# Kernel tuning notes

Measured on AMD Instinct MI355X. Metric: run time of the kernel, lower is better.

The kernel has to match this reference:

```python
import jax, jax.numpy as jnp
import numpy as np

B = 128          # batch
D = 2048         # original_dim
P = 16000        # projection_dim


def _count_sketch_matrix(key, d, p):
    """Dense count-sketch matrix: one +/-1 per row at a random column.
    Mirrors the torch init: col ~ randint(0, p-1), sign = 2*randint(0,2)-1."""
    k_idx, k_sgn = jax.random.split(key)
    idx = jax.random.randint(k_idx, (d,), 0, p - 1)            # torch uses high=p-1 (exclusive)
    sgn = (2 * jax.random.randint(k_sgn, (d,), 0, 2) - 1).astype(jnp.float32)
    C = jnp.zeros((d, p), dtype=jnp.float32)
    return C.at[jnp.arange(d), idx].set(sgn)


def setup_inputs() -> dict:
    key = jax.random.key(0)
    kx1, kx2, kc1, kc2 = jax.random.split(key, 4)
    x1 = jax.random.normal(kx1, (B, D), dtype=jnp.float32)
    x2 = jax.random.normal(kx2, (B, D), dtype=jnp.float32)
    C1 = _count_sketch_matrix(kc1, D, P)
    C2 = _count_sketch_matrix(kc2, D, P)
    return {"x1": x1, "x2": x2, "C1": C1, "C2": C2}


def reference(x1, x2, C1, C2):
    # Count-sketch projections (dense mm, as in the original module)
    y1 = x1 @ C1                      # [B, P]
    y2 = x2 @ C2                      # [B, P]
    # Circular convolution via FFT -> elementwise complex multiply -> IFFT.
    # Original takes only the real part of the IFFT output.
    f1 = jnp.fft.fft(y1, axis=-1)
    f2 = jnp.fft.fft(y2, axis=-1)
    phi = jnp.fft.ifft(f1 * f2, axis=-1).real.astype(jnp.float32)
    return phi                        # [B, P]
```

## Files before the change

### kernel.cpp

```cpp
#include <hip/hip_runtime.h>

#define NFFT 16000
#define BATCH 128
#define DIM 2048

__device__ __forceinline__ float2 cmul(float2 a, float2 b) {
    return make_float2(a.x * b.x - a.y * b.y, a.x * b.y + a.y * b.x);
}

__device__ __forceinline__ int rev5_3(int n) {
    int d0 = n % 5, r = n / 5;
    int d1 = r % 5, d2 = r / 5;
    return d0 * 25 + d1 * 5 + d2;
}

__device__ __forceinline__ int perm_slot(int p) {
    return (p & 127) * 125 + rev5_3(p >> 7);
}

__global__ void gen_twiddles(float2* W) {
    int j = blockIdx.x * blockDim.x + threadIdx.x;
    if (j < NFFT) {
        double a = -2.0 * 3.141592653589793238462643383279502884 * (double)j / (double)NFFT;
        W[j] = make_float2((float)cos(a), (float)sin(a));
    }
}

__global__ void extract_sketch(const float* __restrict__ C1, const float* __restrict__ C2,
                               int* __restrict__ idx1, float* __restrict__ sgn1,
                               int* __restrict__ idx2, float* __restrict__ sgn2) {
    int gwave = (blockIdx.x * blockDim.x + threadIdx.x) >> 6;
    int lane = threadIdx.x & 63;
    if (gwave >= 2 * DIM) return;
    const float* row;
    int* idxp; float* sgnp; int d;
    if (gwave < DIM) { d = gwave;       row = C1 + (size_t)d * NFFT; idxp = idx1; sgnp = sgn1; }
    else             { d = gwave - DIM; row = C2 + (size_t)d * NFFT; idxp = idx2; sgnp = sgn2; }
    for (int it = 0; it < 63; ++it) {
        int off = it * 256 + lane * 4;
        float4 v = make_float4(0.f, 0.f, 0.f, 0.f);
        if (off < NFFT) v = *reinterpret_cast<const float4*>(row + off);
        bool found = (v.x != 0.f) || (v.y != 0.f) || (v.z != 0.f) || (v.w != 0.f);
        if (found) {
            int j; float s;
            if (v.x != 0.f)      { j = 0; s = v.x; }
            else if (v.y != 0.f) { j = 1; s = v.y; }
            else if (v.z != 0.f) { j = 2; s = v.z; }
            else                 { j = 3; s = v.w; }
            idxp[d] = off + j;
            sgnp[d] = s;
        }
        if (__any(found)) break;
    }
}

__device__ void fft16000(float2* ld, const float2* __restrict__ W) {
    const int tid = threadIdx.x;
    const int nt = blockDim.x;
    const float C1_5 = 0.30901699437494742f, S1_5 = 0.95105651629515357f;
    const float C2_5 = -0.80901699437494745f, S2_5 = 0.58778525229247312f;
    const float2 w5tab[5] = { make_float2(1.f, 0.f),
                              make_float2(C1_5, -S1_5), make_float2(C2_5, -S2_5),
                              make_float2(C2_5,  S2_5), make_float2(C1_5,  S1_5) };

    #pragma unroll
    for (int s = 0; s < 3; ++s) {
        const int m = (s == 0) ? 1 : (s == 1) ? 5 : 25;
        const int twmul = NFFT / (5 * m);
        for (int task = tid; task < 128 * 25; task += nt) {
            int n1 = task / 25;
            int bf = task % 25;
            int t = bf % m, blk = bf / m;
            int base = n1 * 125 + blk * (5 * m) + t;
            float2 xv[5];
            #pragma unroll
            for (int r = 0; r < 5; ++r) xv[r] = ld[base + r * m];
            if (m > 1) {
                int step = twmul * t;
                #pragma unroll
                for (int r = 1; r < 5; ++r) xv[r] = cmul(xv[r], W[step * r]);
            }
            float2 y[5];
            #pragma unroll
            for (int q = 0; q < 5; ++q) {
                float2 acc = xv[0];
                #pragma unroll
                for (int r = 1; r < 5; ++r) {
                    float2 t2 = cmul(xv[r], w5tab[(q * r) % 5]);
                    acc.x += t2.x; acc.y += t2.y;
                }
                y[q] = acc;
            }
            #pragma unroll
            for (int q = 0; q < 5; ++q) ld[base + q * m] = y[q];
        }
        __syncthreads();
    }

    for (int idx = tid; idx < NFFT; idx += nt) {
        int n1 = idx / 125;
        int k2 = idx - n1 * 125;
        int rn1 = (int)(__brev((unsigned)n1) >> 25);
        if (n1 > rn1) continue;
        int pb = rn1 * 125 + k2;
        float2 va = ld[idx], vb = ld[pb];
        va = cmul(va, W[n1 * k2]);
        vb = cmul(vb, W[rn1 * k2]);
        ld[idx] = vb;
        ld[pb] = va;
    }
    __syncthreads();

    #pragma unroll
    for (int s = 0; s < 7; ++s) {
        const int m = 1 << s;
        const int twmul = NFFT >> (s + 1);
        for (int task = tid; task < 125 * 64; task += nt) {
            int bf = task / 125;
            int k2 = task - bf * 125;
            int t = bf & (m - 1);
            int blk = bf >> s;
            int pa = (blk * 2 * m + t) * 125 + k2;
            int pb = pa + m * 125;
            float2 a = ld[pa], b = ld[pb];
            float2 wb = cmul(W[twmul * t], b);
            ld[pa] = make_float2(a.x + wb.x, a.y + wb.y);
            ld[pb] = make_float2(a.x - wb.x, a.y - wb.y);
        }
        __syncthreads();
    }
}

__global__ void fused_fft(const float* __restrict__ x1, const float* __restrict__ x2,
                          const int* __restrict__ idx1, const float* __restrict__ sgn1,
                          const int* __restrict__ idx2, const float* __restrict__ sgn2,
                          float* __restrict__ out, const float2* __restrict__ W) {
    extern __shared__ float2 ld[];
    const int b = blockIdx.x;
    const int tid = threadIdx.x, nt = blockDim.x;

    for (int i = tid; i < NFFT; i += nt) ld[i] = make_float2(0.f, 0.f);
    __syncthreads();

    const float* x1b = x1 + (size_t)b * DIM;
    const float* x2b = x2 + (size_t)b * DIM;
    for (int d = tid; d < DIM; d += nt) {
        float v1 = sgn1[d] * x1b[d];
        atomicAdd(&ld[perm_slot(idx1[d])].x, v1);
        float v2 = sgn2[d] * x2b[d];
        atomicAdd(&ld[perm_slot(idx2[d])].y, v2);
    }
    __syncthreads();

    fft16000(ld, W);

    float2 vals[8][2];
    int nk = 0;
    for (int k = tid; k <= NFFT / 2; k += nt) {
        int m = (k == 0) ? 0 : NFFT - k;
        float2 Zk = ld[k], Zm = ld[m];
        float u = (Zk.x * Zk.x - Zk.y * Zk.y) - (Zm.x * Zm.x - Zm.y * Zm.y);
        float v = 2.f * (Zk.x * Zk.y + Zm.x * Zm.y);
        vals[nk][0] = make_float2(0.25f * v,  0.25f * u);
        vals[nk][1] = make_float2(0.25f * v, -0.25f * u);
        ++nk;
    }
    __syncthreads();
    nk = 0;
    for (int k = tid; k <= NFFT / 2; k += nt) {
        ld[perm_slot(k)] = vals[nk][0];
        if (k != 0 && k != NFFT / 2)
            ld[perm_slot(NFFT - k)] = vals[nk][1];
        ++nk;
    }
    __syncthreads();

    fft16000(ld, W);

    const float invN = 1.0f / (float)NFFT;
    float* outb = out + (size_t)b * NFFT;
    for (int k = tid; k < NFFT; k += nt) outb[k] = ld[k].x * invN;
}

extern "C" void kernel_launch(void* const* d_in, const int* in_sizes, int n_in,
                              void* d_out, int out_size, void* d_ws, size_t ws_size,
                              hipStream_t stream) {
    (void)in_sizes; (void)n_in; (void)out_size; (void)ws_size;
    const float* x1 = (const float*)d_in[0];
    const float* x2 = (const float*)d_in[1];
    const float* C1 = (const float*)d_in[2];
    const float* C2 = (const float*)d_in[3];
    float* out = (float*)d_out;

    char* w = (char*)d_ws;
    int*    idx1 = (int*)  (w);
    float*  sgn1 = (float*)(w + 8192);
    int*    idx2 = (int*)  (w + 16384);
    float*  sgn2 = (float*)(w + 24576);
    float2* W    = (float2*)(w + 32768);

    (void)hipFuncSetAttribute((const void*)fused_fft,
                              hipFuncAttributeMaxDynamicSharedMemorySize, NFFT * 8);

    gen_twiddles  <<<63, 256, 0, stream>>>(W);
    extract_sketch<<<(2 * DIM) / 4, 256, 0, stream>>>(C1, C2, idx1, sgn1, idx2, sgn2);
    fused_fft     <<<BATCH, 1024, NFFT * 8, stream>>>(x1, x2, idx1, sgn1, idx2, sgn2, out, W);
}
```

Measured before the change: 356.3 us.

## Restructure FFT into radix-4 stages with on-the-fly twiddles and no reorder pass

Replaces the seven radix-2 stages and the explicit bit-reversal/twiddle permutation pass with three radix-4 stages plus one radix-2 stage, reading output in digit-reversed order via index mapping. Twiddle factors are computed with fast sin/cos intrinsics instead of a global table, removing the twiddle generation kernel. The sketch extraction loads four float4 chunks per step for more memory parallelism. Fast trig intrinsics may reduce accuracy slightly.

```diff
diff --git a/kernel.cpp b/kernel.cpp
--- a/kernel.cpp
+++ b/kernel.cpp
@@ -7,6 +7,9 @@
 __device__ __forceinline__ float2 cmul(float2 a, float2 b) {
     return make_float2(a.x * b.x - a.y * b.y, a.x * b.y + a.y * b.x);
 }
+__device__ __forceinline__ float2 cadd(float2 a, float2 b) { return make_float2(a.x + b.x, a.y + b.y); }
+__device__ __forceinline__ float2 csub(float2 a, float2 b) { return make_float2(a.x - b.x, a.y - b.y); }
+__device__ __forceinline__ float2 cis(float ang) { return make_float2(__cosf(ang), __sinf(ang)); }
 
 __device__ __forceinline__ int rev5_3(int n) {
     int d0 = n % 5, r = n / 5;
@@ -18,12 +21,8 @@
     return (p & 127) * 125 + rev5_3(p >> 7);
 }
 
-__global__ void gen_twiddles(float2* W) {
-    int j = blockIdx.x * blockDim.x + threadIdx.x;
-    if (j < NFFT) {
-        double a = -2.0 * 3.141592653589793238462643383279502884 * (double)j / (double)NFFT;
-        W[j] = make_float2((float)cos(a), (float)sin(a));
-    }
+__device__ __forceinline__ int posn1(int k) {
+    return ((k & 3) << 5) | (((k >> 2) & 3) << 3) | (((k >> 4) & 3) << 1) | (k >> 6);
 }
 
 __global__ void extract_sketch(const float* __restrict__ C1, const float* __restrict__ C2,
@@ -36,27 +35,37 @@
     int* idxp; float* sgnp; int d;
     if (gwave < DIM) { d = gwave;       row = C1 + (size_t)d * NFFT; idxp = idx1; sgnp = sgn1; }
     else             { d = gwave - DIM; row = C2 + (size_t)d * NFFT; idxp = idx2; sgnp = sgn2; }
-    for (int it = 0; it < 63; ++it) {
-        int off = it * 256 + lane * 4;
-        float4 v = make_float4(0.f, 0.f, 0.f, 0.f);
-        if (off < NFFT) v = *reinterpret_cast<const float4*>(row + off);
-        bool found = (v.x != 0.f) || (v.y != 0.f) || (v.z != 0.f) || (v.w != 0.f);
-        if (found) {
-            int j; float s;
-            if (v.x != 0.f)      { j = 0; s = v.x; }
-            else if (v.y != 0.f) { j = 1; s = v.y; }
-            else if (v.z != 0.f) { j = 2; s = v.z; }
-            else                 { j = 3; s = v.w; }
-            idxp[d] = off + j;
-            sgnp[d] = s;
-        }
-        if (__any(found)) break;
-    }
-}
-
-__device__ void fft16000(float2* ld, const float2* __restrict__ W) {
-    const int tid = threadIdx.x;
-    const int nt = blockDim.x;
+    for (int step = 0; step < 16; ++step) {
+        int off0 = step * 1024 + lane * 4;
+        float4 v[4];
+        #pragma unroll
+        for (int c = 0; c < 4; ++c) {
+            int off = off0 + c * 256;
+            v[c] = (off < NFFT) ? *reinterpret_cast<const float4*>(row + off)
+                                : make_float4(0.f, 0.f, 0.f, 0.f);
+        }
+        bool found = false;
+        #pragma unroll
+        for (int c = 0; c < 4; ++c) {
+            float4 w = v[c];
+            if (w.x != 0.f || w.y != 0.f || w.z != 0.f || w.w != 0.f) {
+                int off = off0 + c * 256;
+                int j; float s;
+                if (w.x != 0.f)      { j = 0; s = w.x; }
+                else if (w.y != 0.f) { j = 1; s = w.y; }
+                else if (w.z != 0.f) { j = 2; s = w.z; }
+                else                 { j = 3; s = w.w; }
+                idxp[d] = off + j;
+                sgnp[d] = s;
+                found = true;
+            }
+        }
+        if (__any(found)) return;
+    }
+}
+
+__device__ void fft16000(float2* ld) {
+    const int tid = threadIdx.x, nt = blockDim.x;
     const float C1_5 = 0.30901699437494742f, S1_5 = 0.95105651629515357f;
     const float C2_5 = -0.80901699437494745f, S2_5 = 0.58778525229247312f;
     const float2 w5tab[5] = { make_float2(1.f, 0.f),
@@ -66,19 +75,22 @@
     #pragma unroll
     for (int s = 0; s < 3; ++s) {
         const int m = (s == 0) ? 1 : (s == 1) ? 5 : 25;
-        const int twmul = NFFT / (5 * m);
+        const float angstep = -6.28318530717958647692f / (float)(5 * m);
         for (int task = tid; task < 128 * 25; task += nt) {
             int n1 = task / 25;
-            int bf = task % 25;
+            int bf = task - n1 * 25;
             int t = bf % m, blk = bf / m;
             int base = n1 * 125 + blk * (5 * m) + t;
             float2 xv[5];
             #pragma unroll
             for (int r = 0; r < 5; ++r) xv[r] = ld[base + r * m];
             if (m > 1) {
-                int step = twmul * t;
-                #pragma unroll
-                for (int r = 1; r < 5; ++r) xv[r] = cmul(xv[r], W[step * r]);
+                float2 w1 = cis(angstep * (float)t);
+                float2 w2 = cmul(w1, w1);
+                float2 w3 = cmul(w2, w1);
+                float2 w4 = cmul(w2, w2);
+                xv[1] = cmul(xv[1], w1); xv[2] = cmul(xv[2], w2);
+                xv[3] = cmul(xv[3], w3); xv[4] = cmul(xv[4], w4);
             }
             float2 y[5];
             #pragma unroll
@@ -97,44 +109,99 @@
         __syncthreads();
     }
 
-    for (int idx = tid; idx < NFFT; idx += nt) {
-        int n1 = idx / 125;
-        int k2 = idx - n1 * 125;
-        int rn1 = (int)(__brev((unsigned)n1) >> 25);
-        if (n1 > rn1) continue;
-        int pb = rn1 * 125 + k2;
-        float2 va = ld[idx], vb = ld[pb];
-        va = cmul(va, W[n1 * k2]);
-        vb = cmul(vb, W[rn1 * k2]);
-        ld[idx] = vb;
-        ld[pb] = va;
-    }
-    __syncthreads();
-
-    #pragma unroll
-    for (int s = 0; s < 7; ++s) {
-        const int m = 1 << s;
-        const int twmul = NFFT >> (s + 1);
-        for (int task = tid; task < 125 * 64; task += nt) {
-            int bf = task / 125;
-            int k2 = task - bf * 125;
-            int t = bf & (m - 1);
-            int blk = bf >> s;
-            int pa = (blk * 2 * m + t) * 125 + k2;
-            int pb = pa + m * 125;
+    {
+        const float ANGN = -6.28318530717958647692f / 16000.0f;
+        const float ANGL = -6.28318530717958647692f / 128.0f;
+        for (int tau = tid; tau < 125 * 32; tau += nt) {
+            int j = tau / 125;
+            int k2 = tau - j * 125;
+            float2 v[4];
+            #pragma unroll
+            for (int p = 0; p < 4; ++p) {
+                int n1 = j + 32 * p;
+                float2 x = ld[n1 * 125 + k2];
+                v[p] = cmul(x, cis(ANGN * (float)(n1 * k2)));
+            }
+            float2 s0 = cadd(v[0], v[2]), s1 = cadd(v[1], v[3]);
+            float2 d0 = csub(v[0], v[2]), d1 = csub(v[1], v[3]);
+            float2 t0 = cadd(s0, s1), t2 = csub(s0, s1);
+            float2 t1 = make_float2(d0.x + d1.y, d0.y - d1.x);
+            float2 t3 = make_float2(d0.x - d1.y, d0.y + d1.x);
+            float2 w1 = cis(ANGL * (float)j);
+            float2 w2 = cmul(w1, w1), w3 = cmul(w2, w1);
+            ld[ j       * 125 + k2] = t0;
+            ld[(j + 32) * 125 + k2] = cmul(w1, t1);
+            ld[(j + 64) * 125 + k2] = cmul(w2, t2);
+            ld[(j + 96) * 125 + k2] = cmul(w3, t3);
+        }
+        __syncthreads();
+    }
+    {
+        const float ANGL = -6.28318530717958647692f / 32.0f;
+        for (int tau = tid; tau < 125 * 32; tau += nt) {
+            int bf = tau / 125;
+            int k2 = tau - bf * 125;
+            int j = bf & 7, blk = bf >> 3;
+            int base = blk * 32 + j;
+            float2 v[4];
+            #pragma unroll
+            for (int p = 0; p < 4; ++p) v[p] = ld[(base + 8 * p) * 125 + k2];
+            float2 s0 = cadd(v[0], v[2]), s1 = cadd(v[1], v[3]);
+            float2 d0 = csub(v[0], v[2]), d1 = csub(v[1], v[3]);
+            float2 t0 = cadd(s0, s1), t2 = csub(s0, s1);
+            float2 t1 = make_float2(d0.x + d1.y, d0.y - d1.x);
+            float2 t3 = make_float2(d0.x - d1.y, d0.y + d1.x);
+            float2 w1 = cis(ANGL * (float)j);
+            float2 w2 = cmul(w1, w1), w3 = cmul(w2, w1);
+            ld[(base     ) * 125 + k2] = t0;
+            ld[(base +  8) * 125 + k2] = cmul(w1, t1);
+            ld[(base + 16) * 125 + k2] = cmul(w2, t2);
+            ld[(base + 24) * 125 + k2] = cmul(w3, t3);
+        }
+        __syncthreads();
+    }
+    {
+        const float ANGL = -6.28318530717958647692f / 8.0f;
+        for (int tau = tid; tau < 125 * 32; tau += nt) {
+            int bf = tau / 125;
+            int k2 = tau - bf * 125;
+            int j = bf & 1, blk = bf >> 1;
+            int base = blk * 8 + j;
+            float2 v[4];
+            #pragma unroll
+            for (int p = 0; p < 4; ++p) v[p] = ld[(base + 2 * p) * 125 + k2];
+            float2 s0 = cadd(v[0], v[2]), s1 = cadd(v[1], v[3]);
+            float2 d0 = csub(v[0], v[2]), d1 = csub(v[1], v[3]);
+            float2 t0 = cadd(s0, s1), t2 = csub(s0, s1);
+            float2 t1 = make_float2(d0.x + d1.y, d0.y - d1.x);
+            float2 t3 = make_float2(d0.x - d1.y, d0.y + d1.x);
+            float2 w1 = cis(ANGL * (float)j);
+            float2 w2 = cmul(w1, w1), w3 = cmul(w2, w1);
+            ld[(base    ) * 125 + k2] = t0;
+            ld[(base + 2) * 125 + k2] = cmul(w1, t1);
+            ld[(base + 4) * 125 + k2] = cmul(w2, t2);
+            ld[(base + 6) * 125 + k2] = cmul(w3, t3);
+        }
+        __syncthreads();
+    }
+    {
+        for (int tau = tid; tau < 125 * 64; tau += nt) {
+            int blk = tau / 125;
+            int k2 = tau - blk * 125;
+            int pa = (2 * blk) * 125 + k2, pb = pa + 125;
             float2 a = ld[pa], b = ld[pb];
-            float2 wb = cmul(W[twmul * t], b);
-            ld[pa] = make_float2(a.x + wb.x, a.y + wb.y);
-            ld[pb] = make_float2(a.x - wb.x, a.y - wb.y);
-        }
-        __syncthreads();
-    }
-}
-
-__global__ void fused_fft(const float* __restrict__ x1, const float* __restrict__ x2,
-                          const int* __restrict__ idx1, const float* __restrict__ sgn1,
-                          const int* __restrict__ idx2, const float* __restrict__ sgn2,
-                          float* __restrict__ out, const float2* __restrict__ W) {
+            ld[pa] = cadd(a, b);
+            ld[pb] = csub(a, b);
+        }
+        __syncthreads();
+    }
+}
+
+__global__ void __launch_bounds__(1024)
+fused_fft(const float* __restrict__ x1, const float* __restrict__ x2,
+          const int* __restrict__ idx1, const float* __restrict__ sgn1,
+          const int* __restrict__ idx2, const float* __restrict__ sgn2,
+          float* __restrict__ out) {
     extern __shared__ float2 ld[];
     const int b = blockIdx.x;
     const int tid = threadIdx.x, nt = blockDim.x;
@@ -145,41 +212,44 @@
     const float* x1b = x1 + (size_t)b * DIM;
     const float* x2b = x2 + (size_t)b * DIM;
     for (int d = tid; d < DIM; d += nt) {
-        float v1 = sgn1[d] * x1b[d];
-        atomicAdd(&ld[perm_slot(idx1[d])].x, v1);
-        float v2 = sgn2[d] * x2b[d];
-        atomicAdd(&ld[perm_slot(idx2[d])].y, v2);
-    }
-    __syncthreads();
-
-    fft16000(ld, W);
+        atomicAdd(&ld[perm_slot(idx1[d])].x, sgn1[d] * x1b[d]);
+        atomicAdd(&ld[perm_slot(idx2[d])].y, sgn2[d] * x2b[d]);
+    }
+    __syncthreads();
+
+    fft16000(ld);
 
     float2 vals[8][2];
     int nk = 0;
-    for (int k = tid; k <= NFFT / 2; k += nt) {
-        int m = (k == 0) ? 0 : NFFT - k;
-        float2 Zk = ld[k], Zm = ld[m];
+    for (int k = tid; k <= NFFT / 2; k += nt, ++nk) {
+        int k1 = k / 125, k2 = k - 125 * k1;
+        int k1m, k2m;
+        if (k2 == 0) { k2m = 0;        k1m = (128 - k1) & 127; }
+        else         { k2m = 125 - k2; k1m = 127 - k1; }
+        float2 Zk = ld[posn1(k1)  * 125 + k2];
+        float2 Zm = ld[posn1(k1m) * 125 + k2m];
         float u = (Zk.x * Zk.x - Zk.y * Zk.y) - (Zm.x * Zm.x - Zm.y * Zm.y);
         float v = 2.f * (Zk.x * Zk.y + Zm.x * Zm.y);
         vals[nk][0] = make_float2(0.25f * v,  0.25f * u);
         vals[nk][1] = make_float2(0.25f * v, -0.25f * u);
-        ++nk;
     }
     __syncthreads();
     nk = 0;
-    for (int k = tid; k <= NFFT / 2; k += nt) {
+    for (int k = tid; k <= NFFT / 2; k += nt, ++nk) {
         ld[perm_slot(k)] = vals[nk][0];
         if (k != 0 && k != NFFT / 2)
             ld[perm_slot(NFFT - k)] = vals[nk][1];
-        ++nk;
-    }
-    __syncthreads();
-
-    fft16000(ld, W);
+    }
+    __syncthreads();
+
+    fft16000(ld);
 
     const float invN = 1.0f / (float)NFFT;
     float* outb = out + (size_t)b * NFFT;
-    for (int k = tid; k < NFFT; k += nt) outb[k] = ld[k].x * invN;
+    for (int k = tid; k < NFFT; k += nt) {
+        int k1 = k / 125, k2 = k - 125 * k1;
+        outb[k] = ld[posn1(k1) * 125 + k2].x * invN;
+    }
 }
 
 extern "C" void kernel_launch(void* const* d_in, const int* in_sizes, int n_in,
@@ -197,12 +267,10 @@
     float*  sgn1 = (float*)(w + 8192);
     int*    idx2 = (int*)  (w + 16384);
     float*  sgn2 = (float*)(w + 24576);
-    float2* W    = (float2*)(w + 32768);
 
     (void)hipFuncSetAttribute((const void*)fused_fft,
                               hipFuncAttributeMaxDynamicSharedMemorySize, NFFT * 8);
 
-    gen_twiddles  <<<63, 256, 0, stream>>>(W);
     extract_sketch<<<(2 * DIM) / 4, 256, 0, stream>>>(C1, C2, idx1, sgn1, idx2, sgn2);
-    fused_fft     <<<BATCH, 1024, NFFT * 8, stream>>>(x1, x2, idx1, sgn1, idx2, sgn2, out, W);
-}
+    fused_fft     <<<BATCH, 1024, NFFT * 8, stream>>>(x1, x2, idx1, sgn1, idx2, sgn2, out);
+}
```

New measurement: 320.0 us. -10.2%, faster.
